# Performance work log

Hardware: AMD Instinct MI355X
Metric: run time of the kernel (lower is better)

Reference implementation:

```python
import math
import jax, jax.numpy as jnp
import numpy as np

N_HEADS = 16

def setup_inputs() -> dict:
    key = jax.random.key(0)
    k1, k2, k3 = jax.random.split(key, 3)
    B, T, C = 4, 2048, 1024
    alpha = 0.5
    std = alpha * (1.0 / C) ** 0.5
    x = jax.random.normal(k1, (B, T, C), dtype=jnp.float32)
    w_attn = jax.random.normal(k2, (C, 3 * C), dtype=jnp.float32) * std
    b_attn = jnp.zeros((3 * C,), dtype=jnp.float32)
    w_proj = jax.random.normal(k3, (C, C), dtype=jnp.float32) * std
    b_proj = jnp.zeros((C,), dtype=jnp.float32)
    return {"x": x, "w_attn": w_attn, "b_attn": b_attn, "w_proj": w_proj, "b_proj": b_proj}

def reference(x, w_attn, b_attn, w_proj, b_proj):
    B, T, C = x.shape
    H = N_HEADS
    D = C // H
    qkv = x @ w_attn + b_attn                      # [B,T,3C]
    q, k, v = jnp.split(qkv, 3, axis=-1)
    # [B,T,C] -> [B,H,T,D]
    q = q.reshape(B, T, H, D).transpose(0, 2, 1, 3)
    k = k.reshape(B, T, H, D).transpose(0, 2, 1, 3)
    v = v.reshape(B, T, H, D).transpose(0, 2, 1, 3)
    att = jnp.einsum('bhqd,bhkd->bhqk', q, k) * (1.0 / math.sqrt(D))
    causal = jnp.tril(jnp.ones((T, T), dtype=bool))
    att = jnp.where(causal, att, -jnp.inf)
    att = jax.nn.softmax(att, axis=-1)
    y = jnp.einsum('bhqk,bhkd->bhqd', att, v)      # [B,H,T,D]
    y = y.transpose(0, 2, 1, 3).reshape(B, T, C)
    return y @ w_proj + b_proj
```

## Files before the change

### kernel.cpp

```cpp
#include <hip/hip_runtime.h>
#include <hip/hip_bf16.h>

typedef __bf16 bf16x8 __attribute__((ext_vector_type(8)));
typedef float f32x4 __attribute__((ext_vector_type(4)));
typedef unsigned short u16x8 __attribute__((ext_vector_type(8)));
typedef unsigned short u16x4 __attribute__((ext_vector_type(4)));

#define HB 16
#define TT 2048
#define CCH 1024
#define DD 64

#define AS1 __attribute__((address_space(1)))
#define AS3 __attribute__((address_space(3)))
#define GL16(gp, lp) __builtin_amdgcn_global_load_lds((const AS1 void*)(gp), (AS3 void*)(lp), 16, 0, 0)

__device__ __forceinline__ unsigned short f2bf(float f) {
  union { __hip_bfloat16 h; unsigned short u; } cv;
  cv.h = __float2bfloat16(f);
  return cv.u;
}

__device__ __forceinline__ unsigned pack2(float lo, float hi) {
  return (unsigned)f2bf(lo) | ((unsigned)f2bf(hi) << 16);
}

__device__ __forceinline__ f32x4 mfma16(bf16x8 a, bf16x8 b, f32x4 c) {
  return __builtin_amdgcn_mfma_f32_16x16x32_bf16(a, b, c, 0, 0, 0);
}


__global__ __launch_bounds__(256) void cvt_f32_bf16(const float* __restrict__ in,
                                                    unsigned short* __restrict__ out,
                                                    int n4) {
  int i = blockIdx.x * 256 + threadIdx.x;
  if (i >= n4) return;
  float4 v = reinterpret_cast<const float4*>(in)[i];
  u16x4 o;
  o.x = f2bf(v.x); o.y = f2bf(v.y); o.z = f2bf(v.z); o.w = f2bf(v.w);
  *reinterpret_cast<u16x4*>(out + (size_t)i * 4) = o;
}

__global__ __launch_bounds__(256) void transpose_cvt(const float* __restrict__ w,
                                                     unsigned short* __restrict__ wt,
                                                     int N) {
  __shared__ unsigned short t[32][33];
  int nb = blockIdx.x * 32, kb = blockIdx.y * 32;
  int tx = threadIdx.x & 31, ty = threadIdx.x >> 5;
  #pragma unroll
  for (int r = 0; r < 32; r += 8)
    t[ty + r][tx] = f2bf(w[(size_t)(kb + ty + r) * N + nb + tx]);
  __syncthreads();
  #pragma unroll
  for (int r = 0; r < 32; r += 8)
    wt[(size_t)(nb + ty + r) * 1024 + kb + tx] = t[tx][ty + r];
}


template <int EPI>
__global__ __launch_bounds__(256) void gemm_bf16(
    const unsigned short* __restrict__ A,
    const unsigned short* __restrict__ Bt,
    const float* __restrict__ bias,
    float* __restrict__ outf,
    unsigned short* __restrict__ qb,
    unsigned short* __restrict__ kb,
    unsigned short* __restrict__ vt) {
  __shared__ unsigned short As[8192];
  __shared__ unsigned short Bs[8192];
  const int tid = threadIdx.x;
  const int lane = tid & 63;
  const int wid = tid >> 6;
  const int r16 = lane & 15, g = lane >> 4;
  const int wm = wid >> 1, wn = wid & 1;
  const int m0 = blockIdx.y * 128, n0 = blockIdx.x * 128;
  const int srow = tid >> 3;
  const int schx = (tid & 7) ^ (srow & 7);

  f32x4 acc[4][4];
  #pragma unroll
  for (int i = 0; i < 4; ++i)
    #pragma unroll
    for (int j = 0; j < 4; ++j) acc[i][j] = (f32x4){0.f, 0.f, 0.f, 0.f};

  const int rx = r16 & 7;

  for (int kt = 0; kt < 1024; kt += 64) {
    #pragma unroll
    for (int i = 0; i < 4; ++i) {
      const int row = i * 32 + srow;
      GL16(A + (size_t)(m0 + row) * 1024 + kt + schx * 8, As + i * 2048 + tid * 8);
    }
    #pragma unroll
    for (int i = 0; i < 4; ++i) {
      const int row = i * 32 + srow;
      GL16(Bt + (size_t)(n0 + row) * 1024 + kt + schx * 8, Bs + i * 2048 + tid * 8);
    }
    __syncthreads();
    #pragma unroll
    for (int h = 0; h < 2; ++h) {
      bf16x8 af[4], bfr[4];
      #pragma unroll
      for (int i = 0; i < 4; ++i)
        af[i] = *reinterpret_cast<const bf16x8*>(
            &As[(wm * 64 + i * 16 + r16) * 64 + ((g + 4 * h) ^ rx) * 8]);
      #pragma unroll
      for (int j = 0; j < 4; ++j)
        bfr[j] = *reinterpret_cast<const bf16x8*>(
            &Bs[(wn * 64 + j * 16 + r16) * 64 + ((g + 4 * h) ^ rx) * 8]);
      #pragma unroll
      for (int i = 0; i < 4; ++i)
        #pragma unroll
        for (int j = 0; j < 4; ++j)
          acc[i][j] = mfma16(af[i], bfr[j], acc[i][j]);
    }
    __syncthreads();
  }

  #pragma unroll
  for (int i = 0; i < 4; ++i) {
    #pragma unroll
    for (int j = 0; j < 4; ++j) {
      const int n = n0 + wn * 64 + j * 16 + r16;
      const int mbase = m0 + wm * 64 + i * 16 + g * 4;
      const float bi = bias[n];
      if (EPI == 1) {
        #pragma unroll
        for (int r = 0; r < 4; ++r)
          outf[(size_t)(mbase + r) * 1024 + n] = acc[i][j][r] + bi;
      } else {
        const int which = n >> 10;
        const int cc2 = n & 1023;
        const int h = cc2 >> 6, d = cc2 & 63;
        const int b = mbase >> 11, t = mbase & 2047;
        if (which == 2) {
          u16x4 o;
          #pragma unroll
          for (int r = 0; r < 4; ++r) o[r] = f2bf(acc[i][j][r] + bi);
          *reinterpret_cast<u16x4*>(
              &vt[(((size_t)b * HB + h) * DD + d) * TT + t]) = o;
        } else {
          unsigned short* dst = (which == 0) ? qb : kb;
          const float sc = (which == 0) ? 0.18033688011112042f : 1.0f;
          #pragma unroll
          for (int r = 0; r < 4; ++r)
            dst[(((size_t)b * HB + h) * TT + (t + r)) * DD + d] =
                f2bf((acc[i][j][r] + bi) * sc);
        }
      }
    }
  }
}


__global__ __launch_bounds__(256, 4) void attn_kernel(
    const unsigned short* __restrict__ qg_,
    const unsigned short* __restrict__ kg_,
    const unsigned short* __restrict__ vtg_,
    unsigned short* __restrict__ yb) {
  const int bh = blockIdx.y;
  const int jb = blockIdx.x;
  const int tid = threadIdx.x;
  const int wid = tid >> 6;
  const int lane = tid & 63;
  const int r16 = lane & 15, g = lane >> 4;
  const unsigned short* Q = qg_ + (size_t)bh * TT * DD;
  const unsigned short* K = kg_ + (size_t)bh * TT * DD;
  const unsigned short* Vt = vtg_ + (size_t)bh * DD * TT;
  const int b = bh >> 4, h = bh & 15;

  __shared__ unsigned short smem[2][8192];

  const int krow0 = tid >> 3;
  const int chx = (tid & 7) ^ (krow0 & 7);
  const int rx = r16 & 7;

#define STAGE(bi, kvb_) do {                                                    \
    unsigned short* sb_ = &smem[bi][0];                                         \
    const unsigned short* gk_ = K + (size_t)(kvb_) * DD;                        \
    GL16(gk_ + (size_t)krow0 * DD + chx * 8,               sb_ + tid * 8);      \
    GL16(gk_ + (size_t)(32 + krow0) * DD + chx * 8,        sb_ + 2048 + tid * 8);\
    GL16(Vt + (size_t)krow0 * TT + (kvb_) + chx * 8,       sb_ + 4096 + tid * 8);\
    GL16(Vt + (size_t)(32 + krow0) * TT + (kvb_) + chx * 8, sb_ + 6144 + tid * 8);\
  } while (0)

  #pragma unroll
  for (int part = 0; part < 2; ++part) {
    const int qg0 = (part == 0) ? jb * 64 : (31 - jb) * 64;
    const int nt = (part == 0) ? (jb + 1) : (32 - jb);
    const int qw = qg0 + wid * 16;
    const int q = qw + r16;

    bf16x8 qf0 = *reinterpret_cast<const bf16x8*>(&Q[(size_t)q * DD + g * 8]);
    bf16x8 qf1 = *reinterpret_cast<const bf16x8*>(&Q[(size_t)q * DD + 32 + g * 8]);

    f32x4 yacc[4];
    #pragma unroll
    for (int db = 0; db < 4; ++db) yacc[db] = (f32x4){0.f, 0.f, 0.f, 0.f};
    float m = -1e30f, l = 0.f;

    STAGE(0, 0);
    if (nt > 1) {
      STAGE(1, 64);
      asm volatile("s_waitcnt vmcnt(4)" ::: "memory");
    } else {
      asm volatile("s_waitcnt vmcnt(0)" ::: "memory");
    }
    __builtin_amdgcn_s_barrier();

    for (int t = 0; t < nt; ++t) {
      const int kvb = t * 64;
      const unsigned short* sK = &smem[t & 1][0];
      const unsigned short* sV = &smem[t & 1][4096];

      float s[4][4];
      #pragma unroll
      for (int c = 0; c < 4; ++c) {
        bf16x8 kfa = *reinterpret_cast<const bf16x8*>(
            &sK[(c * 16 + r16) * 64 + (g ^ rx) * 8]);
        bf16x8 kfb = *reinterpret_cast<const bf16x8*>(
            &sK[(c * 16 + r16) * 64 + ((g + 4) ^ rx) * 8]);
        f32x4 z = (f32x4){0.f, 0.f, 0.f, 0.f};
        z = mfma16(kfa, qf0, z);
        z = mfma16(kfb, qf1, z);
        #pragma unroll
        for (int r = 0; r < 4; ++r) s[c][r] = z[r];
      }

      if (t == nt - 1) {
        #pragma unroll
        for (int c = 0; c < 4; ++c)
          #pragma unroll
          for (int r = 0; r < 4; ++r)
            if (kvb + c * 16 + 4 * g + r > q) s[c][r] = -1e30f;
      }
      float mc[4];
      #pragma unroll
      for (int c = 0; c < 4; ++c)
        mc[c] = fmaxf(fmaxf(s[c][0], s[c][1]), fmaxf(s[c][2], s[c][3]));
      float mx = fmaxf(fmaxf(mc[0], mc[1]), fmaxf(mc[2], mc[3]));
      mx = fmaxf(mx, __shfl_xor(mx, 16));
      mx = fmaxf(mx, __shfl_xor(mx, 32));

      if (!__all(mx <= m + 8.f)) {
        const float mn = fmaxf(m, mx);
        const float al = exp2f(m - mn);
        m = mn;
        l *= al;
        #pragma unroll
        for (int db = 0; db < 4; ++db)
          #pragma unroll
          for (int r = 0; r < 4; ++r) yacc[db][r] *= al;
      }
      float sc4[4];
      #pragma unroll
      for (int c = 0; c < 4; ++c) {
        #pragma unroll
        for (int r = 0; r < 4; ++r) s[c][r] = exp2f(s[c][r] - m);
        sc4[c] = (s[c][0] + s[c][1]) + (s[c][2] + s[c][3]);
      }
      float rs = (sc4[0] + sc4[1]) + (sc4[2] + sc4[3]);
      rs += __shfl_xor(rs, 16);
      rs += __shfl_xor(rs, 32);
      l += rs;

      const int s0l = r16 + 16 * ((2 * g) & 3);
      const int s1l = r16 + 16 * ((2 * g + 1) & 3);
      #pragma unroll
      for (int kk = 0; kk < 2; ++kk) {
        const unsigned x0 = pack2(s[2 * kk][0], s[2 * kk][1]);
        const unsigned x1 = pack2(s[2 * kk][2], s[2 * kk][3]);
        const unsigned y0 = pack2(s[2 * kk + 1][0], s[2 * kk + 1][1]);
        const unsigned y1 = pack2(s[2 * kk + 1][2], s[2 * kk + 1][3]);
        unsigned a0 = __shfl((int)x0, s0l, 64);
        unsigned b0 = __shfl((int)y0, s0l, 64);
        unsigned a1 = __shfl((int)x1, s0l, 64);
        unsigned b1 = __shfl((int)y1, s0l, 64);
        unsigned a2 = __shfl((int)x0, s1l, 64);
        unsigned b2 = __shfl((int)y0, s1l, 64);
        unsigned a3 = __shfl((int)x1, s1l, 64);
        unsigned b3 = __shfl((int)y1, s1l, 64);
        union { unsigned w[4]; bf16x8 v; } pf;
        pf.w[0] = (g < 2) ? a0 : b0;
        pf.w[1] = (g < 2) ? a1 : b1;
        pf.w[2] = (g < 2) ? a2 : b2;
        pf.w[3] = (g < 2) ? a3 : b3;
        #pragma unroll
        for (int db = 0; db < 4; ++db) {
          bf16x8 vf = *reinterpret_cast<const bf16x8*>(
              &sV[(db * 16 + r16) * 64 + ((kk * 4 + g) ^ rx) * 8]);
          yacc[db] = mfma16(vf, pf.v, yacc[db]);
        }
      }

      __syncthreads();
      if (t + 2 < nt) STAGE(t & 1, (t + 2) * 64);
    }

    const float rl = 1.0f / l;
    #pragma unroll
    for (int db = 0; db < 4; ++db) {
      u16x4 o;
      #pragma unroll
      for (int r = 0; r < 4; ++r) o[r] = f2bf(yacc[db][r] * rl);
      *reinterpret_cast<u16x4*>(
          &yb[((size_t)b * TT + q) * CCH + h * DD + db * 16 + 4 * g]) = o;
    }
  }
#undef STAGE
}


extern "C" void kernel_launch(void* const* d_in, const int* in_sizes, int n_in,
                              void* d_out, int out_size, void* d_ws, size_t ws_size,
                              hipStream_t stream) {
  const float* x      = (const float*)d_in[0];
  const float* w_attn = (const float*)d_in[1];
  const float* b_attn = (const float*)d_in[2];
  const float* w_proj = (const float*)d_in[3];
  const float* b_proj = (const float*)d_in[4];
  float* out = (float*)d_out;
  char* ws = (char*)d_ws;

  unsigned short* xb  = (unsigned short*)(ws + 0);
  unsigned short* wat = (unsigned short*)(ws + 16777216);
  unsigned short* wpt = (unsigned short*)(ws + 23068672);
  unsigned short* qb  = (unsigned short*)(ws + 25165824);
  unsigned short* kb  = (unsigned short*)(ws + 41943040);
  unsigned short* vt  = (unsigned short*)(ws + 58720256);
  unsigned short* yb  = (unsigned short*)(ws + 75497472);

  cvt_f32_bf16<<<(8192 * 1024 / 4 + 255) / 256, 256, 0, stream>>>(x, xb, 8192 * 1024 / 4);
  transpose_cvt<<<dim3(3072 / 32, 32), 256, 0, stream>>>(w_attn, wat, 3072);
  transpose_cvt<<<dim3(1024 / 32, 32), 256, 0, stream>>>(w_proj, wpt, 1024);

  gemm_bf16<0><<<dim3(3072 / 128, 8192 / 128), 256, 0, stream>>>(
      xb, wat, b_attn, nullptr, qb, kb, vt);

  attn_kernel<<<dim3(16, 4 * HB), 256, 0, stream>>>(qb, kb, vt, yb);

  gemm_bf16<1><<<dim3(1024 / 128, 8192 / 128), 256, 0, stream>>>(
      yb, wpt, b_proj, out, nullptr, nullptr, nullptr);
}
```

Baseline: 199.5 us.

## Triple-buffer attention KV staging with one barrier per tile, add MFMA priority hints

The attention kernel's K/V shared-memory ring grows from two buffers to three. The next-next tile is now issued right after a single barrier at the top of each iteration, replacing the trailing __syncthreads plus a separate barrier, so each tile has one sync instead of two. MFMA sections are wrapped in s_setprio hints, and bf16 packing uses the hardware v_cvt_pk_bf16_f32 instruction instead of scalar conversions. The cost is 16KB more LDS per block, which may lower occupancy under launch_bounds(256,4), plus a redundant extra staging load on the final tiles.

```diff
diff --git a/kernel.cpp b/kernel.cpp
--- a/kernel.cpp
+++ b/kernel.cpp
@@ -22,7 +22,9 @@
 }
 
 __device__ __forceinline__ unsigned pack2(float lo, float hi) {
-  return (unsigned)f2bf(lo) | ((unsigned)f2bf(hi) << 16);
+  unsigned r;
+  asm("v_cvt_pk_bf16_f32 %0, %1, %2" : "=v"(r) : "v"(lo), "v"(hi));
+  return r;
 }
 
 __device__ __forceinline__ f32x4 mfma16(bf16x8 a, bf16x8 b, f32x4 c) {
@@ -169,14 +171,14 @@
   const unsigned short* Vt = vtg_ + (size_t)bh * DD * TT;
   const int b = bh >> 4, h = bh & 15;
 
-  __shared__ unsigned short smem[2][8192];
+  __shared__ unsigned short smem[3][8192];
 
   const int krow0 = tid >> 3;
   const int chx = (tid & 7) ^ (krow0 & 7);
   const int rx = r16 & 7;
 
-#define STAGE(bi, kvb_) do {                                                    \
-    unsigned short* sb_ = &smem[bi][0];                                         \
+#define STAGE(bi_, kvb_) do {                                                   \
+    unsigned short* sb_ = &smem[bi_][0];                                        \
     const unsigned short* gk_ = K + (size_t)(kvb_) * DD;                        \
     GL16(gk_ + (size_t)krow0 * DD + chx * 8,               sb_ + tid * 8);      \
     GL16(gk_ + (size_t)(32 + krow0) * DD + chx * 8,        sb_ + 2048 + tid * 8);\
@@ -200,20 +202,24 @@
     float m = -1e30f, l = 0.f;
 
     STAGE(0, 0);
-    if (nt > 1) {
-      STAGE(1, 64);
+    STAGE(1, (nt > 1 ? 1 : 0) * 64);
+    int bi = 0;
+
+    for (int t = 0; t < nt; ++t) {
       asm volatile("s_waitcnt vmcnt(4)" ::: "memory");
-    } else {
-      asm volatile("s_waitcnt vmcnt(0)" ::: "memory");
-    }
-    __builtin_amdgcn_s_barrier();
-
-    for (int t = 0; t < nt; ++t) {
+      __builtin_amdgcn_s_barrier();
+      {
+        int bs = bi + 2; if (bs >= 3) bs -= 3;
+        const int tn = (t + 2 < nt) ? (t + 2) : (nt - 1);
+        STAGE(bs, tn * 64);
+      }
+
       const int kvb = t * 64;
-      const unsigned short* sK = &smem[t & 1][0];
-      const unsigned short* sV = &smem[t & 1][4096];
+      const unsigned short* sK = &smem[bi][0];
+      const unsigned short* sV = &smem[bi][4096];
 
       float s[4][4];
+      __builtin_amdgcn_s_setprio(1);
       #pragma unroll
       for (int c = 0; c < 4; ++c) {
         bf16x8 kfa = *reinterpret_cast<const bf16x8*>(
@@ -226,6 +232,7 @@
         #pragma unroll
         for (int r = 0; r < 4; ++r) s[c][r] = z[r];
       }
+      __builtin_amdgcn_s_setprio(0);
 
       if (t == nt - 1) {
         #pragma unroll
@@ -285,25 +292,26 @@
         pf.w[1] = (g < 2) ? a1 : b1;
         pf.w[2] = (g < 2) ? a2 : b2;
         pf.w[3] = (g < 2) ? a3 : b3;
+        __builtin_amdgcn_s_setprio(1);
         #pragma unroll
         for (int db = 0; db < 4; ++db) {
           bf16x8 vf = *reinterpret_cast<const bf16x8*>(
               &sV[(db * 16 + r16) * 64 + ((kk * 4 + g) ^ rx) * 8]);
           yacc[db] = mfma16(vf, pf.v, yacc[db]);
         }
-      }
-
-      __syncthreads();
-      if (t + 2 < nt) STAGE(t & 1, (t + 2) * 64);
+        __builtin_amdgcn_s_setprio(0);
+      }
+
+      bi = (bi == 2) ? 0 : bi + 1;
     }
 
     const float rl = 1.0f / l;
     #pragma unroll
     for (int db = 0; db < 4; ++db) {
-      u16x4 o;
-      #pragma unroll
-      for (int r = 0; r < 4; ++r) o[r] = f2bf(yacc[db][r] * rl);
-      *reinterpret_cast<u16x4*>(
+      unsigned w0 = pack2(yacc[db][0] * rl, yacc[db][1] * rl);
+      unsigned w1 = pack2(yacc[db][2] * rl, yacc[db][3] * rl);
+      uint2 o = make_uint2(w0, w1);
+      *reinterpret_cast<uint2*>(
           &yb[((size_t)b * TT + q) * CCH + h * DD + db * 16 + 4 * g]) = o;
     }
   }
```

New measurement: 213.9 us. 1.07x slower.
